# Optimization experiments

Measured on AMD Instinct MI355X. Metric: run time of the kernel, lower is better.

## Reference

```python
import jax, jax.numpy as jnp
import numpy as np

HID = 2048
E = 8          # routed experts
TOP_K = 2
F = 1408       # moe_intermediate_size
FS = 2816      # shared expert intermediate
SCALE = 2.5    # routed_scaling_factor


def setup_inputs() -> dict:
    key = jax.random.key(0)
    ks = jax.random.split(key, 8)
    s = 0.02
    return {
        "hidden_states": jax.random.normal(ks[0], (1, 2048, HID), jnp.float32),
        "w_router": jax.random.normal(ks[1], (HID, E), jnp.float32) * s,
        "w_gate": jax.random.normal(ks[2], (E, HID, F), jnp.float32) * s,
        "w_up": jax.random.normal(ks[3], (E, HID, F), jnp.float32) * s,
        "w_down": jax.random.normal(ks[4], (E, F, HID), jnp.float32) * s,
        "ws_gate": jax.random.normal(ks[5], (HID, FS), jnp.float32) * s,
        "ws_up": jax.random.normal(ks[6], (HID, FS), jnp.float32) * s,
        "ws_down": jax.random.normal(ks[7], (FS, HID), jnp.float32) * s,
    }


def reference(hidden_states, w_router, w_gate, w_up, w_down, ws_gate, ws_up, ws_down):
    B, S, D = hidden_states.shape
    x = hidden_states.reshape(-1, D)                      # [T, D]
    T = x.shape[0]

    # --- router: scores = x @ gate.weight.T (w_router is pre-transposed) ---
    probs = jax.nn.softmax(x @ w_router, axis=-1)         # [T, E]
    top_v, top_i = jax.lax.top_k(probs, TOP_K)            # [T, K]
    top_v = top_v / jnp.sum(top_v, axis=-1, keepdims=True)
    # dense combine weights [T, E] (top-k indices are unique per row)
    combine = jnp.zeros((T, E), x.dtype).at[jnp.arange(T)[:, None], top_i].set(top_v)

    # --- routed experts: SwiGLU MLP per expert, masked combine ---
    g = jax.nn.silu(jnp.einsum("td,edf->etf", x, w_gate))
    u = jnp.einsum("td,edf->etf", x, w_up)
    y = jnp.einsum("etf,efd->etd", g * u, w_down)         # [E, T, D]
    routed = jnp.einsum("etd,te->td", y, combine) * SCALE

    # --- shared experts (always-on SwiGLU MLP) ---
    shared = (jax.nn.silu(x @ ws_gate) * (x @ ws_up)) @ ws_down

    return (routed + shared).reshape(B, S, D)
```

## Files before the change

kernel.cpp:

```cpp
#include <hip/hip_runtime.h>
#include <hip/hip_bf16.h>
#include <stdint.h>

#define TOKS 2048
#define DHID 2048
#define NEXP 8
#define FR 1408
#define FS 2816
#define RSCALE 2.5f

#define G1_SH 352
#define G1_GRID 784
#define G1_Q (G1_GRID / 8)
#define G2_SH 512
#define G2_GRID 1136
#define G2_Q (G2_GRID / 8)
#define NIMG_WG 2816
#define NIMG_WD 2816
#define NIMG_SG 704
#define NIMG_SD 704
#define WIMG_GRID (NIMG_WG*2 + NIMG_WD + NIMG_SG*2 + NIMG_SD)
#define RW_GRID (512 + WIMG_GRID)

typedef float f32x4 __attribute__((ext_vector_type(4)));
typedef short s16x8 __attribute__((ext_vector_type(8)));

__device__ __forceinline__ ushort f2bf(float f) {
  union { __hip_bfloat16 b; ushort u; } v;
  v.b = __float2bfloat16(f);
  return v.u;
}

__device__ __forceinline__ void gload16(const void* g, void* l) {
  __builtin_amdgcn_global_load_lds(
      (const __attribute__((address_space(1))) unsigned int*)g,
      (__attribute__((address_space(3))) unsigned int*)l, 16, 0, 0);
}

__global__ __launch_bounds__(256) void k_rwimg(
    const float* __restrict__ x, const float* __restrict__ wr,
    ushort* __restrict__ xb, int* __restrict__ top_e, float* __restrict__ top_w,
    const float* __restrict__ wg, const float* __restrict__ wu, const float* __restrict__ wd,
    const float* __restrict__ wsg, const float* __restrict__ wsu, const float* __restrict__ wsd,
    ushort* __restrict__ ig, ushort* __restrict__ iu, ushort* __restrict__ id_,
    ushort* __restrict__ isg, ushort* __restrict__ isu, ushort* __restrict__ isd) {
  if (blockIdx.x < 512) {
    const int wid = threadIdx.x >> 6, lane = threadIdx.x & 63;
    const int t = blockIdx.x * 4 + wid;
    const float* xrow = x + (size_t)t * DHID;
    float acc[NEXP];
#pragma unroll
    for (int e = 0; e < NEXP; ++e) acc[e] = 0.f;
#pragma unroll 4
    for (int j = 0; j < DHID / 64; ++j) {
      const int k = j * 64 + lane;
      const float xv = xrow[k];
      xb[(size_t)t * DHID + k] = f2bf(xv);
      const float4 w0 = *(const float4*)(wr + (size_t)k * 8);
      const float4 w1 = *(const float4*)(wr + (size_t)k * 8 + 4);
      acc[0] += xv * w0.x; acc[1] += xv * w0.y; acc[2] += xv * w0.z; acc[3] += xv * w0.w;
      acc[4] += xv * w1.x; acc[5] += xv * w1.y; acc[6] += xv * w1.z; acc[7] += xv * w1.w;
    }
#pragma unroll
    for (int e = 0; e < NEXP; ++e) {
#pragma unroll
      for (int off = 32; off; off >>= 1) acc[e] += __shfl_xor(acc[e], off);
    }
    if (lane == 0) {
      int i1 = 0;
#pragma unroll
      for (int e = 1; e < NEXP; ++e) if (acc[e] > acc[i1]) i1 = e;
      int i2 = (i1 == 0) ? 1 : 0;
#pragma unroll
      for (int e = 0; e < NEXP; ++e) if (e != i1 && acc[e] > acc[i2]) i2 = e;
      const float w1 = 1.f / (1.f + expf(acc[i2] - acc[i1]));
      top_e[2 * t] = i1; top_e[2 * t + 1] = i2;
      top_w[2 * t] = w1; top_w[2 * t + 1] = 1.f - w1;
    }
    return;
  }
  int id = blockIdx.x - 512;
  const float* src; ushort* dst; int N, ntT, ktT;
  if (id < NIMG_WG)                   { src = wg;  dst = ig;  N = FR;   ntT = 11; ktT = 32; }
  else if ((id -= NIMG_WG) < NIMG_WG) { src = wu;  dst = iu;  N = FR;   ntT = 11; ktT = 32; }
  else if ((id -= NIMG_WG) < NIMG_WD) { src = wd;  dst = id_; N = DHID; ntT = 16; ktT = 22; }
  else if ((id -= NIMG_WD) < NIMG_SG) { src = wsg; dst = isg; N = FS;   ntT = 22; ktT = 32; }
  else if ((id -= NIMG_SG) < NIMG_SG) { src = wsu; dst = isu; N = FS;   ntT = 22; ktT = 32; }
  else { id -= NIMG_SG;                 src = wsd; dst = isd; N = DHID; ntT = 16; ktT = 44; }
  const int per_e = ntT * ktT;
  const int e = id / per_e, rem = id % per_e;
  const int nt = rem / ktT, kt = rem % ktT;
  const int K = ktT * 64;
  src += (size_t)e * K * N;
  dst += (size_t)id * 8192;

  __shared__ float lds[64][133];
  const int tid = threadIdx.x;
#pragma unroll
  for (int j = 0; j < 8; ++j) {
    const int idx = j * 256 + tid;
    const int row = idx >> 5, c4 = (idx & 31) << 2;
    const float4 v = *(const float4*)(src + (size_t)(kt * 64 + row) * N + nt * 128 + c4);
    lds[row][c4] = v.x; lds[row][c4 + 1] = v.y; lds[row][c4 + 2] = v.z; lds[row][c4 + 3] = v.w;
  }
  __syncthreads();
#pragma unroll
  for (int s = 0; s < 4; ++s) {
    const int sid = s * 256 + tid;
    const int col = sid >> 3, ks = sid & 7;
    ushort tmp[8];
#pragma unroll
    for (int j = 0; j < 8; ++j) tmp[j] = f2bf(lds[ks * 8 + j][col]);
    *(s16x8*)((char*)dst + col * 128 + ((ks ^ (col & 7)) * 16)) = *(const s16x8*)&tmp[0];
  }
}

__global__ __launch_bounds__(256) void k_lists(
    const int* __restrict__ top_e, const float* __restrict__ top_w,
    int* __restrict__ offs, int* __restrict__ ptok, float* __restrict__ pw,
    int* __restrict__ meta, int* __restrict__ mtl) {
  __shared__ int cnt[NEXP], fill[NEXP], loff[NEXP + 1];
  const int tid = threadIdx.x;
  if (tid < NEXP) { cnt[tid] = 0; fill[tid] = 0; }
  __syncthreads();
  for (int p = tid; p < 2 * TOKS; p += 256) atomicAdd(&cnt[top_e[p]], 1);
  __syncthreads();
  if (tid == 0) {
    loff[0] = 0;
    for (int e = 0; e < NEXP; ++e) loff[e + 1] = loff[e] + cnt[e];
    int n = 0;
    for (int e = 0; e < NEXP; ++e)
      for (int m = 0; m * 128 < cnt[e]; ++m) mtl[n++] = (e << 8) | m;
    meta[0] = n;
  }
  __syncthreads();
  for (int p = tid; p < 2 * TOKS; p += 256) {
    const int e = top_e[p];
    const int pos = loff[e] + atomicAdd(&fill[e], 1);
    ptok[pos] = p >> 1;
    pw[pos] = top_w[p];
  }
  if (tid < NEXP + 1) offs[tid] = loff[tid];
}

__global__ __launch_bounds__(256, 2) void k_gemm1i(
    const ushort* __restrict__ xb,
    const ushort* __restrict__ ig, const ushort* __restrict__ iu, ushort* __restrict__ Hr,
    const ushort* __restrict__ isg, const ushort* __restrict__ isu, ushort* __restrict__ Hs,
    const int* __restrict__ offs, const int* __restrict__ ptok,
    const int* __restrict__ meta, const int* __restrict__ mtl) {
  constexpr int KT = DHID / 64;
  const int swz = (blockIdx.x & 7) * G1_Q + (blockIdx.x >> 3);
  int mt, nt, N, base, count;
  const char *imgG, *imgU;
  ushort* H;
  bool gather;
  if (swz < G1_SH) {
    mt = swz & 15; nt = swz >> 4;
    base = 0; count = TOKS; N = FS;
    imgG = (const char*)isg + (size_t)(nt * 32) * 16384;
    imgU = (const char*)isu + (size_t)(nt * 32) * 16384;
    H = Hs; gather = false;
  } else {
    const int r = swz - G1_SH;
    const int n_mt = meta[0];
    if (r >= n_mt * 11) return;
    const int tile = mtl[r / 11];
    nt = r % 11;
    const int e = tile >> 8; mt = tile & 255;
    base = offs[e]; count = offs[e + 1] - base; N = FR;
    imgG = (const char*)ig + (size_t)((e * 11 + nt) * 32) * 16384;
    imgU = (const char*)iu + (size_t)((e * 11 + nt) * 32) * 16384;
    H = Hr; gather = true;
  }

  __shared__ char smem[81920];
  const int tid = threadIdx.x, lane = tid & 63, wid = tid >> 6;
  const int wm = wid >> 1, wn = wid & 1;

  const int aj = tid & 7;
  const ushort* aptr[4];
  uint32_t alds[4];
#pragma unroll
  for (int i = 0; i < 4; ++i) {
    const int row = i * 32 + (tid >> 3);
    const int gr = mt * 128 + row;
    const int arow = gather ? ptok[base + (gr < count ? gr : count - 1)] : gr;
    aptr[i] = xb + (size_t)arow * DHID + aj * 8;
    alds[i] = (uint32_t)(row * 128 + ((aj ^ (row & 7)) * 16));
  }

  const f32x4 fz = {0.f, 0.f, 0.f, 0.f};
  f32x4 accg[4][4], accu[4][4];
#pragma unroll
  for (int mi = 0; mi < 4; ++mi)
#pragma unroll
    for (int ni = 0; ni < 4; ++ni) { accg[mi][ni] = fz; accu[mi][ni] = fz; }

  s16x8 areg[4];
#pragma unroll
  for (int i = 0; i < 4; ++i) areg[i] = *(const s16x8*)(aptr[i]);
#pragma unroll
  for (int i = 0; i < 4; ++i) {
    const int o = (i * 4 + wid) * 1024 + lane * 16;
    gload16(imgG + o, smem + 16384 + o);
    gload16(imgU + o, smem + 32768 + o);
  }

  for (int t = 0; t < KT; ++t) {
    const int bufo = 16384 + (t & 1) * 32768;
#pragma unroll
    for (int i = 0; i < 4; ++i) *(s16x8*)(smem + alds[i]) = areg[i];
    __builtin_amdgcn_sched_barrier(0);
    if (t + 1 < KT) {
#pragma unroll
      for (int i = 0; i < 4; ++i) areg[i] = *(const s16x8*)(aptr[i] + (t + 1) * 64);
      const int nbufo = 16384 + ((t + 1) & 1) * 32768;
      const char* gG = imgG + (size_t)(t + 1) * 16384;
      const char* gU = imgU + (size_t)(t + 1) * 16384;
#pragma unroll
      for (int i = 0; i < 4; ++i) {
        const int o = (i * 4 + wid) * 1024 + lane * 16;
        gload16(gG + o, smem + nbufo + o);
        gload16(gU + o, smem + nbufo + 16384 + o);
      }
      asm volatile("s_waitcnt vmcnt(20) lgkmcnt(0)" ::: "memory");
    } else {
      asm volatile("s_waitcnt vmcnt(0) lgkmcnt(0)" ::: "memory");
    }
    __builtin_amdgcn_sched_barrier(0);
    __builtin_amdgcn_s_barrier();
    __builtin_amdgcn_sched_barrier(0);
    __builtin_amdgcn_s_setprio(1);
#pragma unroll
    for (int kk = 0; kk < 64; kk += 32) {
      s16x8 af[4];
#pragma unroll
      for (int mi = 0; mi < 4; ++mi) {
        const int row = wm * 64 + mi * 16 + (lane & 15);
        const int slot = (kk >> 3) + (lane >> 4);
        af[mi] = *(const s16x8*)(smem + row * 128 + ((slot ^ (row & 7)) * 16));
      }
#pragma unroll
      for (int ni = 0; ni < 4; ++ni) {
        const int colg = wn * 64 + ni * 16 + (lane & 15);
        const int slot = (kk >> 3) + (lane >> 4);
        const uint32_t boff = (uint32_t)(colg * 128 + ((slot ^ (colg & 7)) * 16));
        const s16x8 bg = *(const s16x8*)(smem + bufo + boff);
        const s16x8 bu = *(const s16x8*)(smem + bufo + 16384 + boff);
#pragma unroll
        for (int mi = 0; mi < 4; ++mi) {
          accg[mi][ni] = __builtin_amdgcn_mfma_f32_16x16x32_bf16(af[mi], bg, accg[mi][ni], 0, 0, 0);
          accu[mi][ni] = __builtin_amdgcn_mfma_f32_16x16x32_bf16(af[mi], bu, accu[mi][ni], 0, 0, 0);
        }
      }
    }
    __builtin_amdgcn_s_setprio(0);
    __builtin_amdgcn_s_barrier();
  }

#pragma unroll
  for (int mi = 0; mi < 4; ++mi) {
    const int gr0 = mt * 128 + wm * 64 + mi * 16 + ((lane >> 4) << 2);
#pragma unroll
    for (int ni = 0; ni < 4; ++ni) {
      const int nc = nt * 128 + wn * 64 + ni * 16 + (lane & 15);
#pragma unroll
      for (int r = 0; r < 4; ++r) {
        const int gr = gr0 + r;
        if (gr < count) {
          const float g = accg[mi][ni][r];
          const float u = accu[mi][ni][r];
          const float h = g / (1.f + __expf(-g)) * u;
          H[(size_t)(base + gr) * N + nc] = f2bf(h);
        }
      }
    }
  }
}

__global__ __launch_bounds__(256, 2) void k_gemm2i(
    const ushort* __restrict__ Hr, const ushort* __restrict__ id_,
    const ushort* __restrict__ Hs, const ushort* __restrict__ isd,
    float* __restrict__ out, const int* __restrict__ offs,
    const int* __restrict__ ptok, const float* __restrict__ pw,
    const int* __restrict__ meta, const int* __restrict__ mtl) {
  constexpr int KT = 22;
  const int swz = (blockIdx.x & 7) * G2_Q + (blockIdx.x >> 3);
  int mt, nt, base, count, K, kofs;
  const ushort* Hbuf;
  const char* img;
  bool routed;
  if (swz < G2_SH) {
    mt = swz & 15; nt = (swz >> 4) & 15;
    const int kh = swz >> 8;
    base = 0; count = TOKS; K = FS; kofs = kh * (KT * 64);
    Hbuf = Hs; img = (const char*)isd + (size_t)(nt * 44 + kh * KT) * 16384;
    routed = false;
  } else {
    const int r = swz - G2_SH;
    const int n_mt = meta[0];
    if (r >= n_mt * 16) return;
    const int tile = mtl[r >> 4];
    nt = r & 15;
    const int e = tile >> 8; mt = tile & 255;
    base = offs[e]; count = offs[e + 1] - base; K = FR; kofs = 0;
    Hbuf = Hr; img = (const char*)id_ + (size_t)((e * 16 + nt) * 22) * 16384;
    routed = true;
  }

  __shared__ char smem[49152];
  const int tid = threadIdx.x, lane = tid & 63, wid = tid >> 6;
  const int wm = wid >> 1, wn = wid & 1;

  const int aj = tid & 7;
  const ushort* aptr[4];
  uint32_t alds[4];
#pragma unroll
  for (int i = 0; i < 4; ++i) {
    const int row = i * 32 + (tid >> 3);
    const int gr = mt * 128 + row;
    const int ar = base + (gr < count ? gr : count - 1);
    aptr[i] = Hbuf + (size_t)ar * K + kofs + aj * 8;
    alds[i] = (uint32_t)(row * 128 + ((aj ^ (row & 7)) * 16));
  }

  const f32x4 fz = {0.f, 0.f, 0.f, 0.f};
  f32x4 acc[4][4];
#pragma unroll
  for (int mi = 0; mi < 4; ++mi)
#pragma unroll
    for (int ni = 0; ni < 4; ++ni) acc[mi][ni] = fz;

  s16x8 areg[4];
#pragma unroll
  for (int i = 0; i < 4; ++i) areg[i] = *(const s16x8*)(aptr[i]);
#pragma unroll
  for (int i = 0; i < 4; ++i) {
    const int o = (i * 4 + wid) * 1024 + lane * 16;
    gload16(img + o, smem + 16384 + o);
  }

  for (int t = 0; t < KT; ++t) {
    const int bufo = 16384 + (t & 1) * 16384;
#pragma unroll
    for (int i = 0; i < 4; ++i) *(s16x8*)(smem + alds[i]) = areg[i];
    __builtin_amdgcn_sched_barrier(0);
    if (t + 1 < KT) {
#pragma unroll
      for (int i = 0; i < 4; ++i) areg[i] = *(const s16x8*)(aptr[i] + (t + 1) * 64);
      const int nbufo = 16384 + ((t + 1) & 1) * 16384;
      const char* gB = img + (size_t)(t + 1) * 16384;
#pragma unroll
      for (int i = 0; i < 4; ++i) {
        const int o = (i * 4 + wid) * 1024 + lane * 16;
        gload16(gB + o, smem + nbufo + o);
      }
      asm volatile("s_waitcnt vmcnt(12) lgkmcnt(0)" ::: "memory");
    } else {
      asm volatile("s_waitcnt vmcnt(0) lgkmcnt(0)" ::: "memory");
    }
    __builtin_amdgcn_sched_barrier(0);
    __builtin_amdgcn_s_barrier();
    __builtin_amdgcn_sched_barrier(0);
    __builtin_amdgcn_s_setprio(1);
#pragma unroll
    for (int kk = 0; kk < 64; kk += 32) {
      s16x8 af[4];
#pragma unroll
      for (int mi = 0; mi < 4; ++mi) {
        const int row = wm * 64 + mi * 16 + (lane & 15);
        const int slot = (kk >> 3) + (lane >> 4);
        af[mi] = *(const s16x8*)(smem + row * 128 + ((slot ^ (row & 7)) * 16));
      }
#pragma unroll
      for (int ni = 0; ni < 4; ++ni) {
        const int colg = wn * 64 + ni * 16 + (lane & 15);
        const int slot = (kk >> 3) + (lane >> 4);
        const uint32_t boff = (uint32_t)(colg * 128 + ((slot ^ (colg & 7)) * 16));
        const s16x8 bb = *(const s16x8*)(smem + bufo + boff);
#pragma unroll
        for (int mi = 0; mi < 4; ++mi)
          acc[mi][ni] = __builtin_amdgcn_mfma_f32_16x16x32_bf16(af[mi], bb, acc[mi][ni], 0, 0, 0);
      }
    }
    __builtin_amdgcn_s_setprio(0);
    __builtin_amdgcn_s_barrier();
  }

#pragma unroll
  for (int mi = 0; mi < 4; ++mi) {
    const int gr0 = mt * 128 + wm * 64 + mi * 16 + ((lane >> 4) << 2);
#pragma unroll
    for (int ni = 0; ni < 4; ++ni) {
      const int nc = nt * 128 + wn * 64 + ni * 16 + (lane & 15);
#pragma unroll
      for (int r = 0; r < 4; ++r) {
        const int gr = gr0 + r;
        if (gr < count) {
          const int arow = base + gr;
          const float s = routed ? (RSCALE * pw[arow]) : 1.f;
          const int tok = routed ? ptok[arow] : gr;
          unsafeAtomicAdd(out + (size_t)tok * DHID + nc, acc[mi][ni][r] * s);
        }
      }
    }
  }
}

extern "C" void kernel_launch(void* const* d_in, const int* in_sizes, int n_in,
                              void* d_out, int out_size, void* d_ws, size_t ws_size,
                              hipStream_t stream) {
  const float* x   = (const float*)d_in[0];
  const float* wr  = (const float*)d_in[1];
  const float* wg  = (const float*)d_in[2];
  const float* wu  = (const float*)d_in[3];
  const float* wd  = (const float*)d_in[4];
  const float* wsg = (const float*)d_in[5];
  const float* wsu = (const float*)d_in[6];
  const float* wsd = (const float*)d_in[7];
  float* out = (float*)d_out;

  uint8_t* p = (uint8_t*)d_ws;
  ushort* xb   = (ushort*)p; p += (size_t)TOKS * DHID * 2;
  int* top_e   = (int*)p;    p += (size_t)2 * TOKS * 4;
  float* top_w = (float*)p;  p += (size_t)2 * TOKS * 4;
  int* offs    = (int*)p;    p += 256;
  int* meta    = (int*)p;    p += 64;
  int* mtl     = (int*)p;    p += 256;
  int* ptok    = (int*)p;    p += (size_t)2 * TOKS * 4;
  float* pw    = (float*)p;  p += (size_t)2 * TOKS * 4;
  ushort* Hr   = (ushort*)p; p += (size_t)2 * TOKS * FR * 2;
  ushort* Hs   = (ushort*)p; p += (size_t)TOKS * FS * 2;
  ushort* ig   = (ushort*)p; p += (size_t)NIMG_WG * 8192 * 2;
  ushort* iu   = (ushort*)p; p += (size_t)NIMG_WG * 8192 * 2;
  ushort* id_  = (ushort*)p; p += (size_t)NIMG_WD * 8192 * 2;
  ushort* isg  = (ushort*)p; p += (size_t)NIMG_SG * 8192 * 2;
  ushort* isu  = (ushort*)p; p += (size_t)NIMG_SG * 8192 * 2;
  ushort* isd  = (ushort*)p; p += (size_t)NIMG_SD * 8192 * 2;

  hipMemsetAsync(d_out, 0, (size_t)out_size * sizeof(float), stream);
  k_rwimg<<<RW_GRID, 256, 0, stream>>>(x, wr, xb, top_e, top_w,
                                       wg, wu, wd, wsg, wsu, wsd,
                                       ig, iu, id_, isg, isu, isd);
  k_lists<<<1, 256, 0, stream>>>(top_e, top_w, offs, ptok, pw, meta, mtl);
  k_gemm1i<<<G1_GRID, 256, 0, stream>>>(xb, ig, iu, Hr, isg, isu, Hs,
                                        offs, ptok, meta, mtl);
  k_gemm2i<<<G2_GRID, 256, 0, stream>>>(Hr, id_, Hs, isd, out,
                                        offs, ptok, pw, meta, mtl);
}
```

Baseline: 401.3 us.

## Load MFMA A-fragments directly from global, drop A staging in LDS, unsplit shared-down K

Both GEMM kernels stop staging the activation A tile through LDS. Each wave now loads its own A fragments straight from global memory into registers in MFMA layout, which shrinks LDS use and removes the LDS stores, LDS reads and the associated lgkmcnt waits. The second GEMM also stops splitting the shared-expert down projection across two K halves, so it launches fewer blocks and does fewer atomic adds, and its launch bound is raised to 4 blocks per CU. The cost is that A rows are now read redundantly across waves straight from global or cache memory without the previous load-ahead, which may expose load latency.

```diff
diff --git a/kernel.cpp b/kernel.cpp
--- a/kernel.cpp
+++ b/kernel.cpp
@@ -12,8 +12,8 @@
 #define G1_SH 352
 #define G1_GRID 784
 #define G1_Q (G1_GRID / 8)
-#define G2_SH 512
-#define G2_GRID 1136
+#define G2_SH 256
+#define G2_GRID 880
 #define G2_Q (G2_GRID / 8)
 #define NIMG_WG 2816
 #define NIMG_WD 2816
@@ -174,20 +174,18 @@
     H = Hr; gather = true;
   }
 
-  __shared__ char smem[81920];
+  __shared__ char smem[65536];
   const int tid = threadIdx.x, lane = tid & 63, wid = tid >> 6;
   const int wm = wid >> 1, wn = wid & 1;
-
-  const int aj = tid & 7;
-  const ushort* aptr[4];
-  uint32_t alds[4];
-#pragma unroll
-  for (int i = 0; i < 4; ++i) {
-    const int row = i * 32 + (tid >> 3);
-    const int gr = mt * 128 + row;
-    const int arow = gather ? ptok[base + (gr < count ? gr : count - 1)] : gr;
-    aptr[i] = xb + (size_t)arow * DHID + aj * 8;
-    alds[i] = (uint32_t)(row * 128 + ((aj ^ (row & 7)) * 16));
+  const int lc = lane & 15, l4 = lane >> 4;
+
+  const ushort* pa[4];
+#pragma unroll
+  for (int mi = 0; mi < 4; ++mi) {
+    const int gr = mt * 128 + wm * 64 + mi * 16 + lc;
+    const int cg = gr < count ? gr : count - 1;
+    const int arow = gather ? ptok[base + cg] : cg;
+    pa[mi] = xb + (size_t)arow * DHID + l4 * 8;
   }
 
   const f32x4 fz = {0.f, 0.f, 0.f, 0.f};
@@ -197,25 +195,24 @@
 #pragma unroll
     for (int ni = 0; ni < 4; ++ni) { accg[mi][ni] = fz; accu[mi][ni] = fz; }
 
-  s16x8 areg[4];
-#pragma unroll
-  for (int i = 0; i < 4; ++i) areg[i] = *(const s16x8*)(aptr[i]);
 #pragma unroll
   for (int i = 0; i < 4; ++i) {
     const int o = (i * 4 + wid) * 1024 + lane * 16;
-    gload16(imgG + o, smem + 16384 + o);
-    gload16(imgU + o, smem + 32768 + o);
+    gload16(imgG + o, smem + o);
+    gload16(imgU + o, smem + 16384 + o);
   }
 
   for (int t = 0; t < KT; ++t) {
-    const int bufo = 16384 + (t & 1) * 32768;
-#pragma unroll
-    for (int i = 0; i < 4; ++i) *(s16x8*)(smem + alds[i]) = areg[i];
+    const int bufo = (t & 1) * 32768;
+    s16x8 af[4][2];
+#pragma unroll
+    for (int mi = 0; mi < 4; ++mi) {
+      af[mi][0] = *(const s16x8*)(pa[mi] + t * 64);
+      af[mi][1] = *(const s16x8*)(pa[mi] + t * 64 + 32);
+    }
     __builtin_amdgcn_sched_barrier(0);
     if (t + 1 < KT) {
-#pragma unroll
-      for (int i = 0; i < 4; ++i) areg[i] = *(const s16x8*)(aptr[i] + (t + 1) * 64);
-      const int nbufo = 16384 + ((t + 1) & 1) * 32768;
+      const int nbufo = ((t + 1) & 1) * 32768;
       const char* gG = imgG + (size_t)(t + 1) * 16384;
       const char* gU = imgU + (size_t)(t + 1) * 16384;
 #pragma unroll
@@ -224,34 +221,27 @@
         gload16(gG + o, smem + nbufo + o);
         gload16(gU + o, smem + nbufo + 16384 + o);
       }
-      asm volatile("s_waitcnt vmcnt(20) lgkmcnt(0)" ::: "memory");
+      asm volatile("s_waitcnt vmcnt(16)" ::: "memory");
     } else {
-      asm volatile("s_waitcnt vmcnt(0) lgkmcnt(0)" ::: "memory");
+      asm volatile("s_waitcnt vmcnt(0)" ::: "memory");
     }
     __builtin_amdgcn_sched_barrier(0);
     __builtin_amdgcn_s_barrier();
     __builtin_amdgcn_sched_barrier(0);
     __builtin_amdgcn_s_setprio(1);
 #pragma unroll
-    for (int kk = 0; kk < 64; kk += 32) {
-      s16x8 af[4];
-#pragma unroll
-      for (int mi = 0; mi < 4; ++mi) {
-        const int row = wm * 64 + mi * 16 + (lane & 15);
-        const int slot = (kk >> 3) + (lane >> 4);
-        af[mi] = *(const s16x8*)(smem + row * 128 + ((slot ^ (row & 7)) * 16));
-      }
+    for (int kk2 = 0; kk2 < 2; ++kk2) {
 #pragma unroll
       for (int ni = 0; ni < 4; ++ni) {
-        const int colg = wn * 64 + ni * 16 + (lane & 15);
-        const int slot = (kk >> 3) + (lane >> 4);
+        const int colg = wn * 64 + ni * 16 + lc;
+        const int slot = kk2 * 4 + l4;
         const uint32_t boff = (uint32_t)(colg * 128 + ((slot ^ (colg & 7)) * 16));
         const s16x8 bg = *(const s16x8*)(smem + bufo + boff);
         const s16x8 bu = *(const s16x8*)(smem + bufo + 16384 + boff);
 #pragma unroll
         for (int mi = 0; mi < 4; ++mi) {
-          accg[mi][ni] = __builtin_amdgcn_mfma_f32_16x16x32_bf16(af[mi], bg, accg[mi][ni], 0, 0, 0);
-          accu[mi][ni] = __builtin_amdgcn_mfma_f32_16x16x32_bf16(af[mi], bu, accu[mi][ni], 0, 0, 0);
+          accg[mi][ni] = __builtin_amdgcn_mfma_f32_16x16x32_bf16(af[mi][kk2], bg, accg[mi][ni], 0, 0, 0);
+          accu[mi][ni] = __builtin_amdgcn_mfma_f32_16x16x32_bf16(af[mi][kk2], bu, accu[mi][ni], 0, 0, 0);
         }
       }
     }
@@ -261,10 +251,10 @@
 
 #pragma unroll
   for (int mi = 0; mi < 4; ++mi) {
-    const int gr0 = mt * 128 + wm * 64 + mi * 16 + ((lane >> 4) << 2);
+    const int gr0 = mt * 128 + wm * 64 + mi * 16 + (l4 << 2);
 #pragma unroll
     for (int ni = 0; ni < 4; ++ni) {
-      const int nc = nt * 128 + wn * 64 + ni * 16 + (lane & 15);
+      const int nc = nt * 128 + wn * 64 + ni * 16 + lc;
 #pragma unroll
       for (int r = 0; r < 4; ++r) {
         const int gr = gr0 + r;
@@ -279,23 +269,21 @@
   }
 }
 
-__global__ __launch_bounds__(256, 2) void k_gemm2i(
+__global__ __launch_bounds__(256, 4) void k_gemm2i(
     const ushort* __restrict__ Hr, const ushort* __restrict__ id_,
     const ushort* __restrict__ Hs, const ushort* __restrict__ isd,
     float* __restrict__ out, const int* __restrict__ offs,
     const int* __restrict__ ptok, const float* __restrict__ pw,
     const int* __restrict__ meta, const int* __restrict__ mtl) {
-  constexpr int KT = 22;
   const int swz = (blockIdx.x & 7) * G2_Q + (blockIdx.x >> 3);
-  int mt, nt, base, count, K, kofs;
+  int mt, nt, base, count, K, KT;
   const ushort* Hbuf;
   const char* img;
   bool routed;
   if (swz < G2_SH) {
-    mt = swz & 15; nt = (swz >> 4) & 15;
-    const int kh = swz >> 8;
-    base = 0; count = TOKS; K = FS; kofs = kh * (KT * 64);
-    Hbuf = Hs; img = (const char*)isd + (size_t)(nt * 44 + kh * KT) * 16384;
+    mt = swz & 15; nt = swz >> 4;
+    base = 0; count = TOKS; K = FS; KT = 44;
+    Hbuf = Hs; img = (const char*)isd + (size_t)(nt * 44) * 16384;
     routed = false;
   } else {
     const int r = swz - G2_SH;
@@ -304,25 +292,22 @@
     const int tile = mtl[r >> 4];
     nt = r & 15;
     const int e = tile >> 8; mt = tile & 255;
-    base = offs[e]; count = offs[e + 1] - base; K = FR; kofs = 0;
+    base = offs[e]; count = offs[e + 1] - base; K = FR; KT = 22;
     Hbuf = Hr; img = (const char*)id_ + (size_t)((e * 16 + nt) * 22) * 16384;
     routed = true;
   }
 
-  __shared__ char smem[49152];
+  __shared__ char smem[32768];
   const int tid = threadIdx.x, lane = tid & 63, wid = tid >> 6;
   const int wm = wid >> 1, wn = wid & 1;
-
-  const int aj = tid & 7;
-  const ushort* aptr[4];
-  uint32_t alds[4];
-#pragma unroll
-  for (int i = 0; i < 4; ++i) {
-    const int row = i * 32 + (tid >> 3);
-    const int gr = mt * 128 + row;
-    const int ar = base + (gr < count ? gr : count - 1);
-    aptr[i] = Hbuf + (size_t)ar * K + kofs + aj * 8;
-    alds[i] = (uint32_t)(row * 128 + ((aj ^ (row & 7)) * 16));
+  const int lc = lane & 15, l4 = lane >> 4;
+
+  const ushort* pa[4];
+#pragma unroll
+  for (int mi = 0; mi < 4; ++mi) {
+    const int gr = mt * 128 + wm * 64 + mi * 16 + lc;
+    const int cg = gr < count ? gr : count - 1;
+    pa[mi] = Hbuf + (size_t)(base + cg) * K + l4 * 8;
   }
 
   const f32x4 fz = {0.f, 0.f, 0.f, 0.f};
@@ -332,56 +317,48 @@
 #pragma unroll
     for (int ni = 0; ni < 4; ++ni) acc[mi][ni] = fz;
 
-  s16x8 areg[4];
-#pragma unroll
-  for (int i = 0; i < 4; ++i) areg[i] = *(const s16x8*)(aptr[i]);
 #pragma unroll
   for (int i = 0; i < 4; ++i) {
     const int o = (i * 4 + wid) * 1024 + lane * 16;
-    gload16(img + o, smem + 16384 + o);
+    gload16(img + o, smem + o);
   }
 
   for (int t = 0; t < KT; ++t) {
-    const int bufo = 16384 + (t & 1) * 16384;
-#pragma unroll
-    for (int i = 0; i < 4; ++i) *(s16x8*)(smem + alds[i]) = areg[i];
+    const int bufo = (t & 1) * 16384;
+    s16x8 af[4][2];
+#pragma unroll
+    for (int mi = 0; mi < 4; ++mi) {
+      af[mi][0] = *(const s16x8*)(pa[mi] + t * 64);
+      af[mi][1] = *(const s16x8*)(pa[mi] + t * 64 + 32);
+    }
     __builtin_amdgcn_sched_barrier(0);
     if (t + 1 < KT) {
-#pragma unroll
-      for (int i = 0; i < 4; ++i) areg[i] = *(const s16x8*)(aptr[i] + (t + 1) * 64);
-      const int nbufo = 16384 + ((t + 1) & 1) * 16384;
+      const int nbufo = ((t + 1) & 1) * 16384;
       const char* gB = img + (size_t)(t + 1) * 16384;
 #pragma unroll
       for (int i = 0; i < 4; ++i) {
         const int o = (i * 4 + wid) * 1024 + lane * 16;
         gload16(gB + o, smem + nbufo + o);
       }
-      asm volatile("s_waitcnt vmcnt(12) lgkmcnt(0)" ::: "memory");
+      asm volatile("s_waitcnt vmcnt(8)" ::: "memory");
     } else {
-      asm volatile("s_waitcnt vmcnt(0) lgkmcnt(0)" ::: "memory");
+      asm volatile("s_waitcnt vmcnt(0)" ::: "memory");
     }
     __builtin_amdgcn_sched_barrier(0);
     __builtin_amdgcn_s_barrier();
     __builtin_amdgcn_sched_barrier(0);
     __builtin_amdgcn_s_setprio(1);
 #pragma unroll
-    for (int kk = 0; kk < 64; kk += 32) {
-      s16x8 af[4];
-#pragma unroll
-      for (int mi = 0; mi < 4; ++mi) {
-        const int row = wm * 64 + mi * 16 + (lane & 15);
-        const int slot = (kk >> 3) + (lane >> 4);
-        af[mi] = *(const s16x8*)(smem + row * 128 + ((slot ^ (row & 7)) * 16));
-      }
+    for (int kk2 = 0; kk2 < 2; ++kk2) {
 #pragma unroll
       for (int ni = 0; ni < 4; ++ni) {
-        const int colg = wn * 64 + ni * 16 + (lane & 15);
-        const int slot = (kk >> 3) + (lane >> 4);
+        const int colg = wn * 64 + ni * 16 + lc;
+        const int slot = kk2 * 4 + l4;
         const uint32_t boff = (uint32_t)(colg * 128 + ((slot ^ (colg & 7)) * 16));
         const s16x8 bb = *(const s16x8*)(smem + bufo + boff);
 #pragma unroll
         for (int mi = 0; mi < 4; ++mi)
-          acc[mi][ni] = __builtin_amdgcn_mfma_f32_16x16x32_bf16(af[mi], bb, acc[mi][ni], 0, 0, 0);
+          acc[mi][ni] = __builtin_amdgcn_mfma_f32_16x16x32_bf16(af[mi][kk2], bb, acc[mi][ni], 0, 0, 0);
       }
     }
     __builtin_amdgcn_s_setprio(0);
@@ -390,10 +367,10 @@
 
 #pragma unroll
   for (int mi = 0; mi < 4; ++mi) {
-    const int gr0 = mt * 128 + wm * 64 + mi * 16 + ((lane >> 4) << 2);
+    const int gr0 = mt * 128 + wm * 64 + mi * 16 + (l4 << 2);
 #pragma unroll
     for (int ni = 0; ni < 4; ++ni) {
-      const int nc = nt * 128 + wn * 64 + ni * 16 + (lane & 15);
+      const int nc = nt * 128 + wn * 64 + ni * 16 + lc;
 #pragma unroll
       for (int r = 0; r < 4; ++r) {
         const int gr = gr0 + r;
```

Result: slower. 520.5 us (+29.7%).

## Make gemm2 waves barrier-free with private B buffers and register A fragments

Applied to the files above, without the earlier changes.

The down-projection GEMM kernel is restructured so each wave loads its own A fragments straight from global memory into registers and streams its own half of the B tile into a private LDS region. This removes the shared A staging and the workgroup barriers. The shared-expert K-split is dropped, so each tile runs all 44 K steps and the grid shrinks. Occupancy is raised to 3 blocks per SM even though LDS grows to 64KB. The gemm1 waitcnt is also changed from 20 to 12, which drains its pipeline more before each step. In exchange, each wave now fetches duplicate A and B data from global memory, and there are fewer blocks to run in parallel.

```diff
diff --git a/kernel.cpp b/kernel.cpp
--- a/kernel.cpp
+++ b/kernel.cpp
@@ -12,8 +12,8 @@
 #define G1_SH 352
 #define G1_GRID 784
 #define G1_Q (G1_GRID / 8)
-#define G2_SH 512
-#define G2_GRID 1136
+#define G2_SH 256
+#define G2_GRID 880
 #define G2_Q (G2_GRID / 8)
 #define NIMG_WG 2816
 #define NIMG_WD 2816
@@ -224,7 +224,7 @@
         gload16(gG + o, smem + nbufo + o);
         gload16(gU + o, smem + nbufo + 16384 + o);
       }
-      asm volatile("s_waitcnt vmcnt(20) lgkmcnt(0)" ::: "memory");
+      asm volatile("s_waitcnt vmcnt(12) lgkmcnt(0)" ::: "memory");
     } else {
       asm volatile("s_waitcnt vmcnt(0) lgkmcnt(0)" ::: "memory");
     }
@@ -279,23 +279,56 @@
   }
 }
 
-__global__ __launch_bounds__(256, 2) void k_gemm2i(
+#define G2STEP(T, CUR, NXT)                                               \
+  {                                                                       \
+    const int bufo_ = ((T) & 1) * 8192;                                   \
+    if ((T) + 1 < KT) {                                                   \
+      _Pragma("unroll") for (int mi = 0; mi < 4; ++mi) {                  \
+        NXT[mi][0] = *(const s16x8*)(pa[mi] + ((T) + 1) * 64);            \
+        NXT[mi][1] = *(const s16x8*)(pa[mi] + ((T) + 1) * 64 + 32);       \
+      }                                                                   \
+      const char* gB_ = img + (size_t)((T) + 1) * 16384 + wn * 8192;      \
+      const int nb_ = (((T) + 1) & 1) * 8192;                             \
+      _Pragma("unroll") for (int i = 0; i < 8; ++i) {                     \
+        const int o_ = i * 1024 + lane * 16;                              \
+        gload16(gB_ + o_, smem + wavebase + nb_ + o_);                    \
+      }                                                                   \
+      asm volatile("s_waitcnt vmcnt(16)" ::: "memory");                   \
+    } else {                                                              \
+      asm volatile("s_waitcnt vmcnt(0)" ::: "memory");                    \
+    }                                                                     \
+    __builtin_amdgcn_sched_barrier(0);                                    \
+    __builtin_amdgcn_s_setprio(1);                                        \
+    _Pragma("unroll") for (int kk2 = 0; kk2 < 2; ++kk2) {                 \
+      _Pragma("unroll") for (int ni = 0; ni < 4; ++ni) {                  \
+        const int c_ = ni * 16 + lc;                                      \
+        const int slot_ = kk2 * 4 + l4;                                   \
+        const uint32_t boff_ = (uint32_t)(wavebase + bufo_ + c_ * 128 +   \
+                                          ((slot_ ^ (c_ & 7)) * 16));     \
+        const s16x8 bb_ = *(const s16x8*)(smem + boff_);                  \
+        _Pragma("unroll") for (int mi = 0; mi < 4; ++mi)                  \
+          acc[mi][ni] = __builtin_amdgcn_mfma_f32_16x16x32_bf16(          \
+              CUR[mi][kk2], bb_, acc[mi][ni], 0, 0, 0);                   \
+      }                                                                   \
+    }                                                                     \
+    __builtin_amdgcn_s_setprio(0);                                        \
+  }
+
+__global__ __launch_bounds__(256, 3) void k_gemm2i(
     const ushort* __restrict__ Hr, const ushort* __restrict__ id_,
     const ushort* __restrict__ Hs, const ushort* __restrict__ isd,
     float* __restrict__ out, const int* __restrict__ offs,
     const int* __restrict__ ptok, const float* __restrict__ pw,
     const int* __restrict__ meta, const int* __restrict__ mtl) {
-  constexpr int KT = 22;
   const int swz = (blockIdx.x & 7) * G2_Q + (blockIdx.x >> 3);
-  int mt, nt, base, count, K, kofs;
+  int mt, nt, base, count, K, KT;
   const ushort* Hbuf;
   const char* img;
   bool routed;
   if (swz < G2_SH) {
-    mt = swz & 15; nt = (swz >> 4) & 15;
-    const int kh = swz >> 8;
-    base = 0; count = TOKS; K = FS; kofs = kh * (KT * 64);
-    Hbuf = Hs; img = (const char*)isd + (size_t)(nt * 44 + kh * KT) * 16384;
+    mt = swz & 15; nt = swz >> 4;
+    base = 0; count = TOKS; K = FS; KT = 44;
+    Hbuf = Hs; img = (const char*)isd + (size_t)(nt * 44) * 16384;
     routed = false;
   } else {
     const int r = swz - G2_SH;
@@ -304,25 +337,23 @@
     const int tile = mtl[r >> 4];
     nt = r & 15;
     const int e = tile >> 8; mt = tile & 255;
-    base = offs[e]; count = offs[e + 1] - base; K = FR; kofs = 0;
+    base = offs[e]; count = offs[e + 1] - base; K = FR; KT = 22;
     Hbuf = Hr; img = (const char*)id_ + (size_t)((e * 16 + nt) * 22) * 16384;
     routed = true;
   }
 
-  __shared__ char smem[49152];
+  __shared__ char smem[65536];
   const int tid = threadIdx.x, lane = tid & 63, wid = tid >> 6;
   const int wm = wid >> 1, wn = wid & 1;
-
-  const int aj = tid & 7;
-  const ushort* aptr[4];
-  uint32_t alds[4];
-#pragma unroll
-  for (int i = 0; i < 4; ++i) {
-    const int row = i * 32 + (tid >> 3);
-    const int gr = mt * 128 + row;
-    const int ar = base + (gr < count ? gr : count - 1);
-    aptr[i] = Hbuf + (size_t)ar * K + kofs + aj * 8;
-    alds[i] = (uint32_t)(row * 128 + ((aj ^ (row & 7)) * 16));
+  const int lc = lane & 15, l4 = lane >> 4;
+  const int wavebase = wid * 16384;
+
+  const ushort* pa[4];
+#pragma unroll
+  for (int mi = 0; mi < 4; ++mi) {
+    const int gr = mt * 128 + wm * 64 + mi * 16 + lc;
+    const int cg = gr < count ? gr : count - 1;
+    pa[mi] = Hbuf + (size_t)(base + cg) * K + l4 * 8;
   }
 
   const f32x4 fz = {0.f, 0.f, 0.f, 0.f};
@@ -332,68 +363,32 @@
 #pragma unroll
     for (int ni = 0; ni < 4; ++ni) acc[mi][ni] = fz;
 
-  s16x8 areg[4];
-#pragma unroll
-  for (int i = 0; i < 4; ++i) areg[i] = *(const s16x8*)(aptr[i]);
-#pragma unroll
-  for (int i = 0; i < 4; ++i) {
-    const int o = (i * 4 + wid) * 1024 + lane * 16;
-    gload16(img + o, smem + 16384 + o);
-  }
-
-  for (int t = 0; t < KT; ++t) {
-    const int bufo = 16384 + (t & 1) * 16384;
-#pragma unroll
-    for (int i = 0; i < 4; ++i) *(s16x8*)(smem + alds[i]) = areg[i];
-    __builtin_amdgcn_sched_barrier(0);
-    if (t + 1 < KT) {
-#pragma unroll
-      for (int i = 0; i < 4; ++i) areg[i] = *(const s16x8*)(aptr[i] + (t + 1) * 64);
-      const int nbufo = 16384 + ((t + 1) & 1) * 16384;
-      const char* gB = img + (size_t)(t + 1) * 16384;
-#pragma unroll
-      for (int i = 0; i < 4; ++i) {
-        const int o = (i * 4 + wid) * 1024 + lane * 16;
-        gload16(gB + o, smem + nbufo + o);
-      }
-      asm volatile("s_waitcnt vmcnt(12) lgkmcnt(0)" ::: "memory");
-    } else {
-      asm volatile("s_waitcnt vmcnt(0) lgkmcnt(0)" ::: "memory");
-    }
-    __builtin_amdgcn_sched_barrier(0);
-    __builtin_amdgcn_s_barrier();
-    __builtin_amdgcn_sched_barrier(0);
-    __builtin_amdgcn_s_setprio(1);
-#pragma unroll
-    for (int kk = 0; kk < 64; kk += 32) {
-      s16x8 af[4];
-#pragma unroll
-      for (int mi = 0; mi < 4; ++mi) {
-        const int row = wm * 64 + mi * 16 + (lane & 15);
-        const int slot = (kk >> 3) + (lane >> 4);
-        af[mi] = *(const s16x8*)(smem + row * 128 + ((slot ^ (row & 7)) * 16));
-      }
-#pragma unroll
-      for (int ni = 0; ni < 4; ++ni) {
-        const int colg = wn * 64 + ni * 16 + (lane & 15);
-        const int slot = (kk >> 3) + (lane >> 4);
-        const uint32_t boff = (uint32_t)(colg * 128 + ((slot ^ (colg & 7)) * 16));
-        const s16x8 bb = *(const s16x8*)(smem + bufo + boff);
-#pragma unroll
-        for (int mi = 0; mi < 4; ++mi)
-          acc[mi][ni] = __builtin_amdgcn_mfma_f32_16x16x32_bf16(af[mi], bb, acc[mi][ni], 0, 0, 0);
-      }
-    }
-    __builtin_amdgcn_s_setprio(0);
-    __builtin_amdgcn_s_barrier();
-  }
-
+  s16x8 af_a[4][2], af_b[4][2];
 #pragma unroll
   for (int mi = 0; mi < 4; ++mi) {
-    const int gr0 = mt * 128 + wm * 64 + mi * 16 + ((lane >> 4) << 2);
+    af_a[mi][0] = *(const s16x8*)(pa[mi]);
+    af_a[mi][1] = *(const s16x8*)(pa[mi] + 32);
+  }
+  {
+    const char* gB = img + wn * 8192;
+#pragma unroll
+    for (int i = 0; i < 8; ++i) {
+      const int o = i * 1024 + lane * 16;
+      gload16(gB + o, smem + wavebase + o);
+    }
+  }
+
+  for (int t = 0; t < KT; t += 2) {
+    G2STEP(t, af_a, af_b);
+    G2STEP(t + 1, af_b, af_a);
+  }
+
+#pragma unroll
+  for (int mi = 0; mi < 4; ++mi) {
+    const int gr0 = mt * 128 + wm * 64 + mi * 16 + (l4 << 2);
 #pragma unroll
     for (int ni = 0; ni < 4; ++ni) {
-      const int nc = nt * 128 + wn * 64 + ni * 16 + (lane & 15);
+      const int nc = nt * 128 + wn * 64 + ni * 16 + lc;
 #pragma unroll
       for (int r = 0; r < 4; ++r) {
         const int gr = gr0 + r;
```

After: 546.2 us. +36.1%, slower.
